# Kernel tuning notes

Measured on AMD Instinct MI355X. Metric: run time of the kernel, lower is better.

Reference implementation:

```python
import jax, jax.numpy as jnp
import numpy as np

B, N, D, Kp = 32, 4096, 128, 256  # batch*heads, seq_len, head_dim, linformer proj dim


def setup_inputs() -> dict:
    key = jax.random.key(0)
    ks = jax.random.split(key, 7)
    return {
        "Q": jax.random.normal(ks[0], (B, N, D), dtype=jnp.float32),
        "K": jax.random.normal(ks[1], (B, N, D), dtype=jnp.float32),
        "V": jax.random.normal(ks[2], (B, N, D), dtype=jnp.float32),
        "E_W": jax.random.normal(ks[3], (Kp, N), dtype=jnp.float32) * (1.0 / np.sqrt(N)),
        "E_b": jax.random.normal(ks[4], (Kp,), dtype=jnp.float32) * 0.02,
        "F_W": jax.random.normal(ks[5], (Kp, N), dtype=jnp.float32) * (1.0 / np.sqrt(N)),
        "F_b": jax.random.normal(ks[6], (Kp,), dtype=jnp.float32) * 0.02,
    }


def reference(Q, K, V, E_W, E_b, F_W, F_b):
    d = Q.shape[-1]
    scale = 1.0 / jnp.sqrt(jnp.asarray(d, Q.dtype))
    # E projection on K^T: [B,d,n] @ W^T -> [B,d,k]
    K_proj = jnp.einsum('bnd,kn->bdk', K, E_W) + E_b  # bias broadcasts over k axis
    # scaled scores [B,n,k], softmax over projected dim k
    scores = jnp.einsum('bnd,bdk->bnk', Q, K_proj) * scale
    P_bar = jax.nn.softmax(scores, axis=-1)
    # F projection on V^T then transpose back: [B,k,d]
    V_proj = jnp.einsum('bnd,kn->bkd', V, F_W) + F_b[:, None]
    # [B,n,k] @ [B,k,d] -> [B,n,d]
    return jnp.einsum('bnk,bkd->bnd', P_bar, V_proj)
```

## Files before the change

### kernel.cpp

```cpp
#include <hip/hip_runtime.h>
#include <cstdint>
#include <cstddef>

#define N_SEQ 4096
#define D_HEAD 128
#define KP_DIM 256

typedef __attribute__((ext_vector_type(4))) float f32x4;
typedef __attribute__((ext_vector_type(8))) short bf16x8;
typedef __attribute__((ext_vector_type(4))) short s16x4;
typedef __attribute__((ext_vector_type(2))) unsigned int u32x2;

static __device__ __forceinline__ short f2bf(float f) {
  uint32_t u = __builtin_bit_cast(uint32_t, f);
  u += 0x7FFFu + ((u >> 16) & 1u);
  return (short)(u >> 16);
}

static __device__ __forceinline__ unsigned int cvtpk(float a, float b) {
  unsigned int r;
  asm("v_cvt_pk_bf16_f32 %0, %1, %2" : "=v"(r) : "v"(a), "v"(b));
  return r;
}

static __device__ __forceinline__ int swz8(int r) { return (r ^ (r >> 2)) & 7; }

__global__ __launch_bounds__(256) void conv_w_kernel(
    const float* __restrict__ EW, const float* __restrict__ FW,
    short* __restrict__ wbf) {
  const int idx = blockIdx.x * 256 + threadIdx.x;
  const int half = 262144;
  f32x4 v = (idx < half) ? *(const f32x4*)(EW + (size_t)idx * 4)
                         : *(const f32x4*)(FW + (size_t)(idx - half) * 4);
  u32x2 h = {cvtpk(v[0], v[1]), cvtpk(v[2], v[3])};
  *(u32x2*)(wbf + (size_t)idx * 4) = h;
}

__global__ __launch_bounds__(512, 4) void proj_partial_kernel(
    const float* __restrict__ Kin, const float* __restrict__ Vin,
    const short* __restrict__ wbf, float* __restrict__ pws) {
  const int bid = blockIdx.x;
  const int wk = (bid & 7) * 64 + (bid >> 3);
  const int kh = wk & 1;
  const int b = (wk >> 1) & 31;
  const int s = (wk >> 6) & 3;
  const int p = wk >> 8;

  const float* __restrict__ X = (p == 0 ? Kin : Vin) + (size_t)b * (N_SEQ * D_HEAD);
  const short* __restrict__ wp =
      wbf + (size_t)p * (KP_DIM * N_SEQ) + (size_t)(kh * 128) * N_SEQ;
  float* __restrict__ outp = pws + ((((size_t)b * 2 + p) * 4) + s) * (KP_DIM * D_HEAD)
                             + (size_t)(kh * 128) * D_HEAD;

  __shared__ __align__(16) short lw[2][128 * 64];
  __shared__ __align__(16) short xt[2][128 * 64];

  const int t = threadIdx.x;
  const int lane = t & 63;
  const int w = t >> 6;
  const int wkk = (w >> 1) * 32;
  const int wdd = (w & 1) * 64;
  const int l15 = lane & 15;
  const int l4 = lane >> 4;
  const int dq = t & 31;
  const int ng = t >> 5;

  const int n0 = s * 1024;

  f32x4 acc[2][4];
#pragma unroll
  for (int i = 0; i < 2; ++i)
#pragma unroll
    for (int j = 0; j < 4; ++j) acc[i][j] = (f32x4){0.f, 0.f, 0.f, 0.f};

  f32x4 xA[4], xB[4];

#define PROJ_WISSUE(BUF, NC)                                                        \
  do {                                                                              \
    _Pragma("unroll") for (int i_ = 0; i_ < 2; ++i_) {                              \
      int g_ = t + i_ * 512;                                                        \
      int row_ = g_ >> 3, c_ = g_ & 7;                                              \
      __builtin_amdgcn_global_load_lds(                                             \
          (const __attribute__((address_space(1))) void*)(wp + (size_t)row_ * N_SEQ \
              + (NC) + ((c_ ^ swz8(row_)) << 3)),                                   \
          (__attribute__((address_space(3))) void*)(&lw[BUF][g_ * 8]), 16, 0, 0);   \
    }                                                                               \
  } while (0)

#define PROJ_XISSUE(XR, NC)                                                         \
  do {                                                                              \
    _Pragma("unroll") for (int i_ = 0; i_ < 4; ++i_)                                \
      XR[i_] = *(const f32x4*)(X + (size_t)((NC) + ng * 4 + i_) * D_HEAD + dq * 4); \
  } while (0)

#define PROJ_XCVT(XR, BUF)                                                          \
  do {                                                                              \
    _Pragma("unroll") for (int j_ = 0; j_ < 4; ++j_) {                              \
      int drow_ = dq * 4 + j_;                                                      \
      u32x2 hv_ = {cvtpk(XR[0][j_], XR[1][j_]), cvtpk(XR[2][j_], XR[3][j_])};       \
      *(u32x2*)(&xt[BUF][drow_ * 64 + ((ng * 4) ^ (swz8(drow_) << 3))]) = hv_;      \
    }                                                                               \
  } while (0)

#define PROJ_COMPUTE(CUR)                                                           \
  do {                                                                              \
    _Pragma("unroll") for (int ks2 = 0; ks2 < 2; ++ks2) {                           \
      const int col0 = ks2 * 32 + l4 * 8;                                           \
      bf16x8 a_[2], bb_[4];                                                         \
      _Pragma("unroll") for (int mt = 0; mt < 2; ++mt) {                            \
        int row_ = wkk + mt * 16 + l15;                                             \
        a_[mt] = *(const bf16x8*)(&lw[CUR][row_ * 64 + (col0 ^ (swz8(row_) << 3))]); \
      }                                                                             \
      _Pragma("unroll") for (int nt = 0; nt < 4; ++nt) {                            \
        int row_ = wdd + nt * 16 + l15;                                             \
        bb_[nt] = *(const bf16x8*)(&xt[CUR][row_ * 64 + (col0 ^ (swz8(row_) << 3))]); \
      }                                                                             \
      _Pragma("unroll") for (int mt = 0; mt < 2; ++mt)                              \
        _Pragma("unroll") for (int nt = 0; nt < 4; ++nt)                            \
          acc[mt][nt] = __builtin_amdgcn_mfma_f32_16x16x32_bf16(a_[mt], bb_[nt],    \
                                                                acc[mt][nt], 0, 0, 0); \
    }                                                                               \
  } while (0)

  PROJ_XISSUE(xA, n0);
  PROJ_WISSUE(0, n0);
  asm volatile("s_waitcnt vmcnt(2)" ::: "memory");
  PROJ_XCVT(xA, 0);
  PROJ_XISSUE(xB, n0 + 64);
  asm volatile("s_waitcnt vmcnt(4)" ::: "memory");
  __syncthreads();

  for (int itp = 0; itp < 7; ++itp) {
    const int it0 = itp * 2;
    PROJ_WISSUE(1, n0 + (it0 + 1) * 64);
    PROJ_XISSUE(xA, n0 + (it0 + 2) * 64);
    PROJ_COMPUTE(0);
    asm volatile("s_waitcnt vmcnt(6)" ::: "memory");
    PROJ_XCVT(xB, 1);
    asm volatile("s_waitcnt vmcnt(4)" ::: "memory");
    __syncthreads();
    PROJ_WISSUE(0, n0 + (it0 + 2) * 64);
    PROJ_XISSUE(xB, n0 + (it0 + 3) * 64);
    PROJ_COMPUTE(1);
    asm volatile("s_waitcnt vmcnt(6)" ::: "memory");
    PROJ_XCVT(xA, 0);
    asm volatile("s_waitcnt vmcnt(4)" ::: "memory");
    __syncthreads();
  }
  PROJ_WISSUE(1, n0 + 15 * 64);
  PROJ_COMPUTE(0);
  asm volatile("s_waitcnt vmcnt(2)" ::: "memory");
  PROJ_XCVT(xB, 1);
  asm volatile("s_waitcnt vmcnt(0)" ::: "memory");
  __syncthreads();
  PROJ_COMPUTE(1);

#undef PROJ_WISSUE
#undef PROJ_XISSUE
#undef PROJ_XCVT
#undef PROJ_COMPUTE

#pragma unroll
  for (int mt = 0; mt < 2; ++mt)
#pragma unroll
    for (int nt = 0; nt < 4; ++nt)
#pragma unroll
      for (int r = 0; r < 4; ++r) {
        int kk = wkk + mt * 16 + l4 * 4 + r;
        int dd = wdd + nt * 16 + l15;
        outp[kk * D_HEAD + dd] = acc[mt][nt][r];
      }
}

__global__ __launch_bounds__(256) void reduce_bias_kernel(
    const float* __restrict__ pws, const float* __restrict__ Eb,
    const float* __restrict__ Fb, short* __restrict__ kp, short* __restrict__ vpt) {
  const int sub = blockIdx.x & 3;
  const int b = blockIdx.x >> 2;
  const int t = threadIdx.x;
  __shared__ short tile[128 * 128];
  if (sub < 2) {
    const float* __restrict__ base = pws + ((size_t)b * 2) * 4 * 32768;
    const int off = sub * 16384;
    for (int i = t; i < 16384; i += 256) {
      int ii = off + i;
      int k = ii >> 7;
      float v = base[ii] + base[ii + 32768] + base[ii + 65536] + base[ii + 98304] + Eb[k];
      kp[(size_t)b * 32768 + ii] = f2bf(v);
    }
  } else {
    const int kh = sub - 2;
    const float* __restrict__ base = pws + (((size_t)b * 2 + 1) * 4) * 32768 + kh * 16384;
    for (int i = t; i < 16384; i += 256) {
      int kl = i >> 7, d = i & 127;
      float v = base[i] + base[i + 32768] + base[i + 65536] + base[i + 98304] + Fb[kh * 128 + kl];
      tile[kl * 128 + (d ^ ((kl & 15) << 3))] = f2bf(v);
    }
    __syncthreads();
    for (int i = t; i < 16384; i += 256) {
      int d = i >> 7, kl = i & 127;
      vpt[(size_t)b * 32768 + d * 256 + kh * 128 + kl] = tile[kl * 128 + (d ^ ((kl & 15) << 3))];
    }
  }
}

__global__ __launch_bounds__(1024, 4) void attn_kernel(
    const float* __restrict__ Q, const short* __restrict__ kp,
    const short* __restrict__ vpt, float* __restrict__ out) {
  const int bid = blockIdx.x;
  const int wk = (bid & 7) * 32 + (bid >> 3);
  const int b = wk >> 3;
  const int slice = wk & 7;
  const int t = threadIdx.x;
  const int lane = t & 63;
  const int w = t >> 6;
  const int l15 = lane & 15, l4 = lane >> 4;

  __shared__ __align__(16) short lbuf[81920];
  short* lkp = lbuf;
  short* lvpt = lbuf + 32768;
  short* lpw = lbuf + 65536 + w * 1024;

  const short* __restrict__ kpb = kp + (size_t)b * 32768;
  const short* __restrict__ vptb = vpt + (size_t)b * 32768;

#pragma unroll
  for (int i = 0; i < 4; ++i) {
    int g = t + i * 1024;
    int row = g >> 4, c = g & 15;
    __builtin_amdgcn_global_load_lds(
        (const __attribute__((address_space(1))) void*)(kpb + (size_t)row * 128 +
                                                        ((c ^ (row & 7)) << 3)),
        (__attribute__((address_space(3))) void*)(&lkp[g * 8]), 16, 0, 0);
  }
#pragma unroll
  for (int i = 0; i < 4; ++i) {
    int g = t + i * 1024;
    int row = g >> 5, c = g & 31;
    __builtin_amdgcn_global_load_lds(
        (const __attribute__((address_space(1))) void*)(vptb + (size_t)row * 256 +
                                                        ((c ^ (row & 7)) << 3)),
        (__attribute__((address_space(3))) void*)(&lvpt[g * 8]), 16, 0, 0);
  }

  const float scale = 0.08838834764831845f;
  f32x4 qraw[8];
  {
    const float* qr = Q + ((size_t)b * N_SEQ + slice * 512 + w * 16 + l15) * D_HEAD;
#pragma unroll
    for (int ks = 0; ks < 4; ++ks) {
      qraw[2 * ks] = *(const f32x4*)(qr + ks * 32 + l4 * 8);
      qraw[2 * ks + 1] = *(const f32x4*)(qr + ks * 32 + l4 * 8 + 4);
    }
  }
  asm volatile("s_waitcnt vmcnt(0)" ::: "memory");
  __syncthreads();

#pragma unroll
  for (int rd = 0; rd < 2; ++rd) {
    const int rowBase = slice * 512 + rd * 256 + w * 16;

    bf16x8 qf[4];
#pragma unroll
    for (int ks = 0; ks < 4; ++ks) {
      union { unsigned int u[4]; bf16x8 v; } cv;
      cv.u[0] = cvtpk(qraw[2 * ks][0] * scale, qraw[2 * ks][1] * scale);
      cv.u[1] = cvtpk(qraw[2 * ks][2] * scale, qraw[2 * ks][3] * scale);
      cv.u[2] = cvtpk(qraw[2 * ks + 1][0] * scale, qraw[2 * ks + 1][1] * scale);
      cv.u[3] = cvtpk(qraw[2 * ks + 1][2] * scale, qraw[2 * ks + 1][3] * scale);
      qf[ks] = cv.v;
    }

    f32x4 accs[16];
#pragma unroll
    for (int i = 0; i < 16; ++i) accs[i] = (f32x4){0.f, 0.f, 0.f, 0.f};
#pragma unroll
    for (int ks = 0; ks < 4; ++ks) {
#pragma unroll
      for (int nt = 0; nt < 16; ++nt) {
        bf16x8 af = *(const bf16x8*)(&lkp[(nt * 16 + l15) * 128 +
                                          (((ks * 4 + l4) ^ (l15 & 7)) << 3)]);
        accs[nt] = __builtin_amdgcn_mfma_f32_16x16x32_bf16(af, qf[ks], accs[nt], 0, 0, 0);
      }
    }

    float m = -1e30f;
#pragma unroll
    for (int nt = 0; nt < 16; ++nt)
#pragma unroll
      for (int r = 0; r < 4; ++r) m = fmaxf(m, accs[nt][r]);
    m = fmaxf(m, __shfl_xor(m, 16));
    m = fmaxf(m, __shfl_xor(m, 32));
    float s = 0.f;
#pragma unroll
    for (int nt = 0; nt < 16; ++nt)
#pragma unroll
      for (int r = 0; r < 4; ++r) {
        float e = __expf(accs[nt][r] - m);
        accs[nt][r] = e;
        s += e;
      }
    s += __shfl_xor(s, 16);
    s += __shfl_xor(s, 32);
    float inv = 1.0f / s;

    f32x4 acco[8];
#pragma unroll
    for (int i = 0; i < 8; ++i) acco[i] = (f32x4){0.f, 0.f, 0.f, 0.f};
#pragma unroll
    for (int qq = 0; qq < 4; ++qq) {
#pragma unroll
      for (int ntl = 0; ntl < 4; ++ntl) {
        int nt = qq * 4 + ntl;
        int cw = 2 * ntl + (l4 >> 1);
        unsigned int p0 = cvtpk(accs[nt][0] * inv, accs[nt][1] * inv);
        unsigned int p1 = cvtpk(accs[nt][2] * inv, accs[nt][3] * inv);
        *(u32x2*)((char*)lpw + l15 * 128 + ((cw ^ (l15 & 7)) << 4) + (l4 & 1) * 8) =
            (u32x2){p0, p1};
      }
      if (rd == 0 && qq == 3) {
        const float* qr = Q + ((size_t)b * N_SEQ + slice * 512 + 256 + w * 16 + l15) * D_HEAD;
#pragma unroll
        for (int ks = 0; ks < 4; ++ks) {
          qraw[2 * ks] = *(const f32x4*)(qr + ks * 32 + l4 * 8);
          qraw[2 * ks + 1] = *(const f32x4*)(qr + ks * 32 + l4 * 8 + 4);
        }
      }
#pragma unroll
      for (int ksl = 0; ksl < 2; ++ksl) {
        bf16x8 pa = *(const bf16x8*)((char*)lpw + l15 * 128 +
                                     (((4 * ksl + l4) ^ (l15 & 7)) << 4));
        int ksa = qq * 2 + ksl;
#pragma unroll
        for (int ntv = 0; ntv < 8; ++ntv) {
          bf16x8 av = *(const bf16x8*)(&lvpt[(ntv * 16 + l15) * 256 +
                                             (((ksa * 4 + l4) ^ (l15 & 7)) << 3)]);
          acco[ntv] = __builtin_amdgcn_mfma_f32_16x16x32_bf16(av, pa, acco[ntv], 0, 0, 0);
        }
      }
    }

    float* ob = out + ((size_t)b * N_SEQ + rowBase) * D_HEAD;
#pragma unroll
    for (int ntv = 0; ntv < 8; ++ntv)
      *(f32x4*)(ob + (size_t)l15 * D_HEAD + ntv * 16 + l4 * 4) = acco[ntv];
  }
}

extern "C" void kernel_launch(void* const* d_in, const int* in_sizes, int n_in,
                              void* d_out, int out_size, void* d_ws, size_t ws_size,
                              hipStream_t stream) {
  const float* Q  = (const float*)d_in[0];
  const float* K  = (const float*)d_in[1];
  const float* V  = (const float*)d_in[2];
  const float* EW = (const float*)d_in[3];
  const float* Eb = (const float*)d_in[4];
  const float* FW = (const float*)d_in[5];
  const float* Fb = (const float*)d_in[6];
  float* out = (float*)d_out;

  short* wbf = (short*)d_out;
  float* pws = (float*)d_out + 2097152;
  short* kpb = (short*)d_ws;
  short* vpt = (short*)((char*)d_ws + (size_t)32 * KP_DIM * D_HEAD * 2);

  conv_w_kernel<<<dim3(2048), dim3(256), 0, stream>>>(EW, FW, wbf);
  proj_partial_kernel<<<dim3(512), dim3(512), 0, stream>>>(K, V, wbf, pws);
  reduce_bias_kernel<<<dim3(128), dim3(256), 0, stream>>>(pws, Eb, Fb, kpb, vpt);
  attn_kernel<<<dim3(256), dim3(1024), 0, stream>>>(Q, kpb, vpt, out);
}
```

Baseline: 100.0 us.

## Split projection blocks along head dim instead of projected dim

Each projection block now covers all 256 projected rows for a 64-column half of the head dimension, instead of 128 projected rows for all 128 head columns. The aim is for each fp32 K/V tile to be loaded and converted to bf16 by exactly one block, removing the duplicated conversion work. In exchange, the bf16 weight tile per step doubles to 256x64, which raises the LDS footprint and weight traffic. The wait counts are adjusted to match the new mix of 4 weight loads and 2 activation loads per thread.

```diff
diff --git a/kernel.cpp b/kernel.cpp
--- a/kernel.cpp
+++ b/kernel.cpp
@@ -8,7 +8,6 @@
 
 typedef __attribute__((ext_vector_type(4))) float f32x4;
 typedef __attribute__((ext_vector_type(8))) short bf16x8;
-typedef __attribute__((ext_vector_type(4))) short s16x4;
 typedef __attribute__((ext_vector_type(2))) unsigned int u32x2;
 
 static __device__ __forceinline__ short f2bf(float f) {
@@ -41,29 +40,28 @@
     const short* __restrict__ wbf, float* __restrict__ pws) {
   const int bid = blockIdx.x;
   const int wk = (bid & 7) * 64 + (bid >> 3);
-  const int kh = wk & 1;
+  const int dh = wk & 1;
   const int b = (wk >> 1) & 31;
   const int s = (wk >> 6) & 3;
   const int p = wk >> 8;
 
-  const float* __restrict__ X = (p == 0 ? Kin : Vin) + (size_t)b * (N_SEQ * D_HEAD);
-  const short* __restrict__ wp =
-      wbf + (size_t)p * (KP_DIM * N_SEQ) + (size_t)(kh * 128) * N_SEQ;
+  const float* __restrict__ X =
+      (p == 0 ? Kin : Vin) + (size_t)b * (N_SEQ * D_HEAD) + dh * 64;
+  const short* __restrict__ wp = wbf + (size_t)p * (KP_DIM * N_SEQ);
   float* __restrict__ outp = pws + ((((size_t)b * 2 + p) * 4) + s) * (KP_DIM * D_HEAD)
-                             + (size_t)(kh * 128) * D_HEAD;
-
-  __shared__ __align__(16) short lw[2][128 * 64];
-  __shared__ __align__(16) short xt[2][128 * 64];
+                             + dh * 64;
+
+  __shared__ __align__(16) short lw[2][KP_DIM * 64];
+  __shared__ __align__(16) short xt[2][64 * 64];
 
   const int t = threadIdx.x;
   const int lane = t & 63;
   const int w = t >> 6;
-  const int wkk = (w >> 1) * 32;
-  const int wdd = (w & 1) * 64;
+  const int wkk = w * 32;
   const int l15 = lane & 15;
   const int l4 = lane >> 4;
-  const int dq = t & 31;
-  const int ng = t >> 5;
+  const int dq = t & 15;
+  const int rp = t >> 4;
 
   const int n0 = s * 1024;
 
@@ -73,11 +71,11 @@
 #pragma unroll
     for (int j = 0; j < 4; ++j) acc[i][j] = (f32x4){0.f, 0.f, 0.f, 0.f};
 
-  f32x4 xA[4], xB[4];
+  f32x4 xA[2], xB[2];
 
 #define PROJ_WISSUE(BUF, NC)                                                        \
   do {                                                                              \
-    _Pragma("unroll") for (int i_ = 0; i_ < 2; ++i_) {                              \
+    _Pragma("unroll") for (int i_ = 0; i_ < 4; ++i_) {                              \
       int g_ = t + i_ * 512;                                                        \
       int row_ = g_ >> 3, c_ = g_ & 7;                                              \
       __builtin_amdgcn_global_load_lds(                                             \
@@ -89,16 +87,16 @@
 
 #define PROJ_XISSUE(XR, NC)                                                         \
   do {                                                                              \
-    _Pragma("unroll") for (int i_ = 0; i_ < 4; ++i_)                                \
-      XR[i_] = *(const f32x4*)(X + (size_t)((NC) + ng * 4 + i_) * D_HEAD + dq * 4); \
+    _Pragma("unroll") for (int i_ = 0; i_ < 2; ++i_)                                \
+      XR[i_] = *(const f32x4*)(X + (size_t)((NC) + rp * 2 + i_) * D_HEAD + dq * 4); \
   } while (0)
 
 #define PROJ_XCVT(XR, BUF)                                                          \
   do {                                                                              \
     _Pragma("unroll") for (int j_ = 0; j_ < 4; ++j_) {                              \
       int drow_ = dq * 4 + j_;                                                      \
-      u32x2 hv_ = {cvtpk(XR[0][j_], XR[1][j_]), cvtpk(XR[2][j_], XR[3][j_])};       \
-      *(u32x2*)(&xt[BUF][drow_ * 64 + ((ng * 4) ^ (swz8(drow_) << 3))]) = hv_;      \
+      unsigned int hv_ = cvtpk(XR[0][j_], XR[1][j_]);                               \
+      *(unsigned int*)(&xt[BUF][drow_ * 64 + ((rp * 2) ^ (swz8(drow_) << 3))]) = hv_; \
     }                                                                               \
   } while (0)
 
@@ -107,27 +105,27 @@
     _Pragma("unroll") for (int ks2 = 0; ks2 < 2; ++ks2) {                           \
       const int col0 = ks2 * 32 + l4 * 8;                                           \
       bf16x8 a_[2], bb_[4];                                                         \
-      _Pragma("unroll") for (int mt = 0; mt < 2; ++mt) {                            \
-        int row_ = wkk + mt * 16 + l15;                                             \
-        a_[mt] = *(const bf16x8*)(&lw[CUR][row_ * 64 + (col0 ^ (swz8(row_) << 3))]); \
+      _Pragma("unroll") for (int mt_ = 0; mt_ < 2; ++mt_) {                         \
+        int row_ = wkk + mt_ * 16 + l15;                                            \
+        a_[mt_] = *(const bf16x8*)(&lw[CUR][row_ * 64 + (col0 ^ (swz8(row_) << 3))]); \
       }                                                                             \
-      _Pragma("unroll") for (int nt = 0; nt < 4; ++nt) {                            \
-        int row_ = wdd + nt * 16 + l15;                                             \
-        bb_[nt] = *(const bf16x8*)(&xt[CUR][row_ * 64 + (col0 ^ (swz8(row_) << 3))]); \
+      _Pragma("unroll") for (int nt_ = 0; nt_ < 4; ++nt_) {                         \
+        int row_ = nt_ * 16 + l15;                                                  \
+        bb_[nt_] = *(const bf16x8*)(&xt[CUR][row_ * 64 + (col0 ^ (swz8(row_) << 3))]); \
       }                                                                             \
-      _Pragma("unroll") for (int mt = 0; mt < 2; ++mt)                              \
-        _Pragma("unroll") for (int nt = 0; nt < 4; ++nt)                            \
-          acc[mt][nt] = __builtin_amdgcn_mfma_f32_16x16x32_bf16(a_[mt], bb_[nt],    \
-                                                                acc[mt][nt], 0, 0, 0); \
+      _Pragma("unroll") for (int mt_ = 0; mt_ < 2; ++mt_)                           \
+        _Pragma("unroll") for (int nt_ = 0; nt_ < 4; ++nt_)                         \
+          acc[mt_][nt_] = __builtin_amdgcn_mfma_f32_16x16x32_bf16(a_[mt_], bb_[nt_], \
+                                                                  acc[mt_][nt_], 0, 0, 0); \
     }                                                                               \
   } while (0)
 
   PROJ_XISSUE(xA, n0);
   PROJ_WISSUE(0, n0);
-  asm volatile("s_waitcnt vmcnt(2)" ::: "memory");
+  asm volatile("s_waitcnt vmcnt(4)" ::: "memory");
   PROJ_XCVT(xA, 0);
   PROJ_XISSUE(xB, n0 + 64);
-  asm volatile("s_waitcnt vmcnt(4)" ::: "memory");
+  asm volatile("s_waitcnt vmcnt(2)" ::: "memory");
   __syncthreads();
 
   for (int itp = 0; itp < 7; ++itp) {
@@ -137,19 +135,19 @@
     PROJ_COMPUTE(0);
     asm volatile("s_waitcnt vmcnt(6)" ::: "memory");
     PROJ_XCVT(xB, 1);
-    asm volatile("s_waitcnt vmcnt(4)" ::: "memory");
+    asm volatile("s_waitcnt vmcnt(2)" ::: "memory");
     __syncthreads();
     PROJ_WISSUE(0, n0 + (it0 + 2) * 64);
     PROJ_XISSUE(xB, n0 + (it0 + 3) * 64);
     PROJ_COMPUTE(1);
     asm volatile("s_waitcnt vmcnt(6)" ::: "memory");
     PROJ_XCVT(xA, 0);
-    asm volatile("s_waitcnt vmcnt(4)" ::: "memory");
+    asm volatile("s_waitcnt vmcnt(2)" ::: "memory");
     __syncthreads();
   }
   PROJ_WISSUE(1, n0 + 15 * 64);
   PROJ_COMPUTE(0);
-  asm volatile("s_waitcnt vmcnt(2)" ::: "memory");
+  asm volatile("s_waitcnt vmcnt(4)" ::: "memory");
   PROJ_XCVT(xB, 1);
   asm volatile("s_waitcnt vmcnt(0)" ::: "memory");
   __syncthreads();
@@ -167,7 +165,7 @@
 #pragma unroll
       for (int r = 0; r < 4; ++r) {
         int kk = wkk + mt * 16 + l4 * 4 + r;
-        int dd = wdd + nt * 16 + l15;
+        int dd = nt * 16 + l15;
         outp[kk * D_HEAD + dd] = acc[mt][nt][r];
       }
 }
```

Measured after the change: 95.87 us. -4.1%, faster.
